# Kernel optimization log

Measured on AMD Instinct MI355X. Metric: run time of the kernel, lower is better.

## Reference

```python
import jax, jax.numpy as jnp
import numpy as np

B, T, C = 4, 2048, 1024
E, I, K = 8, 1408, 2
N_SHARED = 1
IS = I * N_SHARED  # shared expert intermediate size


def setup_inputs() -> dict:
    key = jax.random.key(0)
    ks = jax.random.split(key, 8)
    s = 0.02
    return {
        "x": jax.random.normal(ks[0], (B, T, C), dtype=jnp.float32),
        "Wg": jax.random.normal(ks[1], (E, C), dtype=jnp.float32) * s,   # gate: Linear(C->E), weight [out,in]
        "W1": jax.random.normal(ks[2], (E, I, C), dtype=jnp.float32) * s,  # fc_1 per expert
        "W2": jax.random.normal(ks[3], (E, I, C), dtype=jnp.float32) * s,  # fc_2 per expert
        "W3": jax.random.normal(ks[4], (E, C, I), dtype=jnp.float32) * s,  # proj per expert
        "Ws1": jax.random.normal(ks[5], (IS, C), dtype=jnp.float32) * s,   # shared expert fc_1
        "Ws2": jax.random.normal(ks[6], (IS, C), dtype=jnp.float32) * s,   # shared expert fc_2
        "Ws3": jax.random.normal(ks[7], (C, IS), dtype=jnp.float32) * s,   # shared expert proj
    }


def reference(x, Wg, W1, W2, W3, Ws1, Ws2, Ws3):
    b, t, c = x.shape
    xf = x.reshape(-1, c)                       # [N, C]
    n = xf.shape[0]

    # Router: softmax in float32, top-k gating
    logits = xf @ Wg.T                          # [N, E]
    probs = jax.nn.softmax(logits.astype(jnp.float32), axis=-1)
    topk_p, topk_i = jax.lax.top_k(probs, K)    # [N, K]
    topk_p = topk_p.astype(x.dtype)

    # Dense combine weights: w[n, e] = sum_k topk_p[n, k] * (topk_i[n, k] == e)
    comb = jnp.zeros((n, E), dtype=x.dtype).at[jnp.arange(n)[:, None], topk_i].add(topk_p)

    # All experts on all tokens (dense equivalent of masked dispatch), weighted combine
    g = jnp.einsum('nc,eic->nei', xf, W1)       # [N, E, I]
    u = jnp.einsum('nc,eic->nei', xf, W2)       # [N, E, I]
    h = jax.nn.silu(g) * u                      # SwiGLU
    o = jnp.einsum('nei,eci->nec', h, W3)       # [N, E, C]
    y = jnp.einsum('nec,ne->nc', o, comb).reshape(b, t, c)

    # Shared expert on the residual input
    shared = (jax.nn.silu(x @ Ws1.T) * (x @ Ws2.T)) @ Ws3.T  # [B, T, C]
    return y + shared
```

## Files before the change

kernel.cpp:

```cpp
#include <hip/hip_runtime.h>
#include <stdint.h>

typedef __bf16 bf16;
typedef __attribute__((ext_vector_type(8))) __bf16 bf16x8;
typedef __attribute__((ext_vector_type(4))) float f32x4;

#define N_TOK 8192
#define C_DIM 1024
#define I_DIM 1408
#define NE 8
#define NEA 9
#define H_ROWS 25600

#define CNT_OFF   0
#define OFFS_OFF  64
#define TT_OFF    128
#define BTOK_OFF  192
#define BP_OFF    (BTOK_OFF + NE * N_TOK * 4)
#define ROUTER_END (BP_OFF + NE * N_TOK * 4)
#define TSEL_OFF  ROUTER_END
#define TP0_OFF   (TSEL_OFF + N_TOK * 4)
#define TP1_OFF   (TP0_OFF + N_TOK * 4)
#define XB_OFF    (1u << 20)
#define WB1_OFF   (18u << 20)
#define WB2_OFF   (43u << 20)
#define WB3_OFF   (68u << 20)
#define H_OFF     (93u << 20)

__device__ __forceinline__ void gload16(const void* g, void* l) {
  __builtin_amdgcn_global_load_lds(
      (const __attribute__((address_space(1))) void*)g,
      (__attribute__((address_space(3))) void*)l, 16, 0, 0);
}

__device__ __forceinline__ void vmw(int sel) {
  if (sel == 8) asm volatile("s_waitcnt vmcnt(8)" ::: "memory");
  else asm volatile("s_waitcnt vmcnt(0)" ::: "memory");
}

#define SCHED() __builtin_amdgcn_sched_barrier(0)

#define PHASE(BASE, HALF, READB, STAGEBLK, VMSEL)                              \
  {                                                                            \
    if (READB) {                                                               \
      _Pragma("unroll") for (int nf = 0; nf < 4; ++nf)                         \
          bv[nf] = *(const bf16x8*)((BASE) + 16384 + boff[nf]);                \
    }                                                                          \
    _Pragma("unroll") for (int q = 0; q < 4; ++q)                              \
        av[q] = *(const bf16x8*)((BASE) + aoff[(HALF)*4 + q]);                 \
    STAGEBLK;                                                                  \
    SCHED();                                                                   \
    __builtin_amdgcn_s_barrier();                                              \
    asm volatile("s_waitcnt lgkmcnt(0)" ::: "memory");                         \
    SCHED();                                                                   \
    __builtin_amdgcn_s_setprio(1);                                             \
    _Pragma("unroll") for (int q = 0; q < 4; ++q)                              \
        _Pragma("unroll") for (int nf = 0; nf < 4; ++nf)                       \
            acc[(HALF)*4 + q][nf] = __builtin_amdgcn_mfma_f32_16x16x32_bf16(   \
                av[q], bv[nf], acc[(HALF)*4 + q][nf], 0, 0, 0);                \
    __builtin_amdgcn_s_setprio(0);                                             \
    SCHED();                                                                   \
    if ((VMSEL) >= 0) vmw(VMSEL);                                              \
    __builtin_amdgcn_s_barrier();                                              \
    SCHED();                                                                   \
  }

__global__ __launch_bounds__(256) void convert_kernel(
    const float* __restrict__ src, bf16* __restrict__ dst, int n8) {
  int i = blockIdx.x * 256 + threadIdx.x;
  if (i >= n8) return;
  const float* s = src + (size_t)i * 8;
  float4 a = *(const float4*)(s);
  float4 b = *(const float4*)(s + 4);
  bf16x8 v;
  v[0] = (bf16)a.x; v[1] = (bf16)a.y; v[2] = (bf16)a.z; v[3] = (bf16)a.w;
  v[4] = (bf16)b.x; v[5] = (bf16)b.y; v[6] = (bf16)b.z; v[7] = (bf16)b.w;
  *(bf16x8*)(dst + (size_t)i * 8) = v;
}

__global__ __launch_bounds__(256) void logits_kernel(
    const float* __restrict__ x, const float* __restrict__ Wg,
    int* __restrict__ tsel, float* __restrict__ tp0, float* __restrict__ tp1) {
  __shared__ __align__(16) float wg[NE * C_DIM];
  int t = threadIdx.x;
#pragma unroll
  for (int j = 0; j < 8; ++j) {
    int idx = (t + 256 * j) * 4;
    *(float4*)&wg[idx] = *(const float4*)&Wg[idx];
  }
  __syncthreads();
  int wid = t >> 6, lane = t & 63;
  int tok = blockIdx.x * 4 + wid;
  const float* xr = x + (size_t)tok * C_DIM;
  float acc[NE];
#pragma unroll
  for (int e = 0; e < NE; ++e) acc[e] = 0.f;
#pragma unroll
  for (int j = 0; j < 4; ++j) {
    int c4 = (lane + 64 * j) * 4;
    float4 xv = *(const float4*)&xr[c4];
#pragma unroll
    for (int e = 0; e < NE; ++e) {
      float4 wv = *(const float4*)&wg[e * C_DIM + c4];
      acc[e] += xv.x * wv.x + xv.y * wv.y + xv.z * wv.z + xv.w * wv.w;
    }
  }
  for (int o = 32; o >= 1; o >>= 1)
#pragma unroll
    for (int e = 0; e < NE; ++e) acc[e] += __shfl_xor(acc[e], o, 64);
  if (lane == 0) {
    float m = acc[0];
#pragma unroll
    for (int e = 1; e < NE; ++e) m = fmaxf(m, acc[e]);
    float p[NE], s = 0.f;
#pragma unroll
    for (int e = 0; e < NE; ++e) { p[e] = __expf(acc[e] - m); s += p[e]; }
    float inv = 1.f / s;
#pragma unroll
    for (int e = 0; e < NE; ++e) p[e] *= inv;
    int e0 = 0; float p0 = p[0];
#pragma unroll
    for (int e = 1; e < NE; ++e) if (p[e] > p0) { p0 = p[e]; e0 = e; }
    int e1 = -1; float p1 = -1.f;
#pragma unroll
    for (int e = 0; e < NE; ++e) {
      if (e == e0) continue;
      if (p[e] > p1) { p1 = p[e]; e1 = e; }
    }
    tsel[tok] = e0 | (e1 << 8);
    tp0[tok] = p0;
    tp1[tok] = p1;
  }
}

__global__ __launch_bounds__(1024) void bucketize_kernel(
    const int* __restrict__ tsel, const float* __restrict__ tp0,
    const float* __restrict__ tp1, int* __restrict__ cnt,
    int* __restrict__ btok, float* __restrict__ bp) {
  int e = blockIdx.x;
  int t = threadIdx.x;
  __shared__ int psum[1024];
  int sel[8], loc[8];
  int cntloc = 0;
  int base_tok = t * 8;
#pragma unroll
  for (int j = 0; j < 8; ++j) {
    int s = tsel[base_tok + j];
    int hit = ((s & 0xff) == e) ? 1 : ((((s >> 8) & 0xff) == e) ? 2 : 0);
    sel[j] = hit;
    loc[j] = cntloc;
    cntloc += (hit != 0);
  }
  psum[t] = cntloc;
  __syncthreads();
  for (int off = 1; off < 1024; off <<= 1) {
    int v = (t >= off) ? psum[t - off] : 0;
    __syncthreads();
    psum[t] += v;
    __syncthreads();
  }
  int excl = psum[t] - cntloc;
  if (t == 1023) cnt[e] = psum[1023];
#pragma unroll
  for (int j = 0; j < 8; ++j) {
    if (sel[j]) {
      int pos = excl + loc[j];
      int tok = base_tok + j;
      btok[e * N_TOK + pos] = tok;
      bp[e * N_TOK + pos] = (sel[j] == 1) ? tp0[tok] : tp1[tok];
    }
  }
}

__global__ void offsets_kernel(const int* __restrict__ cnt, int* __restrict__ offs,
                               int* __restrict__ tt) {
  if (threadIdx.x == 0) {
    int a = 0, b = 0;
    for (int e = 0; e < NE; ++e) {
      offs[e] = a; tt[e] = b;
      int pad = (cnt[e] + 127) & ~127;
      a += pad;
      b += (pad + 255) >> 8;
    }
    offs[NE] = a; tt[NE] = b;
  }
}

__device__ __forceinline__ int swz_off(int row, int kg) {
  return row * 64 + ((kg ^ ((row >> 1) & 3)) * 16);
}

__global__ __launch_bounds__(512) void stage1_kernel(
    const bf16* __restrict__ xb, const bf16* __restrict__ wb1,
    const bf16* __restrict__ wb2, const int* __restrict__ cnt,
    const int* __restrict__ offs, const int* __restrict__ tt,
    const int* __restrict__ btok, bf16* __restrict__ H) {
  int bid = blockIdx.x;
  int wgid = (bid & 7) * 154 + (bid >> 3);
  int tau = wgid % 112;
  int i0 = (wgid / 112) * 128;
  int e, row0, slotbase, limit;
  if (tau < 32) {
    e = NE; row0 = tau * 256; slotbase = 0; limit = N_TOK;
  } else {
    int tr = tau - 32;
    if (tr >= tt[NE]) return;
    e = NE - 1;
#pragma unroll
    for (int q = 0; q < NE; ++q) if (tr < tt[q + 1]) { e = q; break; }
    row0 = (tr - tt[e]) * 256;
    slotbase = N_TOK + offs[e];
    limit = cnt[e];
    if (row0 >= limit) return;
  }

  __shared__ __align__(16) char smem[131072];
  const int t = threadIdx.x;
  const int lane = t & 63, wid = t >> 6;
  const int wr = wid >> 2, wc = wid & 3;
  const int l15 = lane & 15, l4 = lane >> 4;

  const int srow = t >> 2;
  const int gsrc = (t & 3) ^ ((srow >> 1) & 3);
  int ar0 = row0 + srow, ar1 = row0 + srow + 128;
  int tok0, tok1;
  if (e == NE) { tok0 = ar0; tok1 = ar1; }
  else {
    int ix0 = e * N_TOK + (ar0 < N_TOK ? ar0 : N_TOK - 1);
    int ix1 = e * N_TOK + (ar1 < N_TOK ? ar1 : N_TOK - 1);
    tok0 = btok[ix0] & (N_TOK - 1);
    tok1 = btok[ix1] & (N_TOK - 1);
  }
  const bf16* asrc0 = xb + (size_t)tok0 * C_DIM + gsrc * 8;
  const bf16* asrc1 = xb + (size_t)tok1 * C_DIM + gsrc * 8;
  const bf16* bsrc0;
  const bf16* bsrc1;
  {
    int r = srow;
    int q = r >> 4, m = q >> 1, sel = q & 1;
    int irow = i0 + m * 16 + (r & 15);
    bsrc0 = (sel ? wb2 : wb1) + ((size_t)e * I_DIM + irow) * C_DIM + gsrc * 8;
    r = srow + 128;
    q = r >> 4; m = q >> 1; sel = q & 1;
    irow = i0 + m * 16 + (r & 15);
    bsrc1 = (sel ? wb2 : wb1) + ((size_t)e * I_DIM + irow) * C_DIM + gsrc * 8;
  }
  const int lo0 = t * 16;
  const int NKT = C_DIM / 32;

  auto stA = [&](int z) {
    if (z < NKT) {
      char* d = smem + (z & 3) * 32768;
      int k = z * 32;
      gload16(asrc0 + k, d + lo0);
      gload16(asrc1 + k, d + 8192 + lo0);
    }
  };
  auto stB = [&](int z) {
    if (z < NKT) {
      char* d = smem + (z & 3) * 32768 + 16384;
      int k = z * 32;
      gload16(bsrc0 + k, d + lo0);
      gload16(bsrc1 + k, d + 8192 + lo0);
    }
  };

  int aoff[8], boff[4];
#pragma unroll
  for (int mf = 0; mf < 8; ++mf) aoff[mf] = swz_off(wr * 128 + mf * 16 + l15, l4);
#pragma unroll
  for (int nf = 0; nf < 4; ++nf) boff[nf] = swz_off(wc * 64 + nf * 16 + l15, l4);

  f32x4 acc[8][4];
  f32x4 zero = {0.f, 0.f, 0.f, 0.f};
#pragma unroll
  for (int mf = 0; mf < 8; ++mf)
#pragma unroll
    for (int nf = 0; nf < 4; ++nf) acc[mf][nf] = zero;
  bf16x8 av[4], bv[4];

  stB(0); stA(0); stB(1); stA(1); stB(2); stA(2);
  asm volatile("s_waitcnt vmcnt(0)" ::: "memory");
  __builtin_amdgcn_s_barrier();
  SCHED();

  const int NIT = NKT / 2;
  for (int it = 0; it < NIT; ++it) {
    char* q0 = smem + ((2 * it) & 3) * 32768;
    char* q1 = smem + ((2 * it + 1) & 3) * 32768;
    int zB = 2 * it + 3, zC = 2 * it + 4;
    int v1 = (zB < NKT) ? 8 : 0;
    int v2 = (zC < NKT) ? 8 : 0;
    PHASE(q0, 0, 1, { stB(zB); }, -1);
    PHASE(q0, 1, 0, { stA(zB); }, v1);
    PHASE(q1, 0, 1, { stB(zC); }, -1);
    PHASE(q1, 1, 0, { stA(zC); }, v2);
  }

#pragma unroll
  for (int mf = 0; mf < 8; ++mf)
#pragma unroll
    for (int r = 0; r < 4; ++r) {
      int rr = row0 + wr * 128 + mf * 16 + l4 * 4 + r;
      if (rr < limit) {
#pragma unroll
        for (int p = 0; p < 2; ++p) {
          float g = acc[mf][2 * p][r];
          float u = acc[mf][2 * p + 1][r];
          float h = (g / (1.f + __expf(-g))) * u;
          int col = i0 + (wc * 2 + p) * 16 + l15;
          H[(size_t)(slotbase + rr) * I_DIM + col] = (bf16)h;
        }
      }
    }
}

template <int SHARED>
__global__ __launch_bounds__(512) void stage2_kernel(
    const bf16* __restrict__ H, const bf16* __restrict__ wb3,
    const int* __restrict__ cnt, const int* __restrict__ offs,
    const int* __restrict__ tt, const int* __restrict__ btok,
    const float* __restrict__ bp, float* __restrict__ y) {
  int bid = blockIdx.x;
  int e, row0, slotbase, limit, c0;
  if (SHARED) {
    int wgid = (bid & 7) * 16 + (bid >> 3);
    e = NE; row0 = (wgid % 32) * 256; slotbase = 0; limit = N_TOK;
    c0 = (wgid / 32) * 256;
  } else {
    int wgid = (bid & 7) * 40 + (bid >> 3);
    int tr = wgid % 80;
    c0 = (wgid / 80) * 256;
    if (tr >= tt[NE]) return;
    e = NE - 1;
#pragma unroll
    for (int q = 0; q < NE; ++q) if (tr < tt[q + 1]) { e = q; break; }
    row0 = (tr - tt[e]) * 256;
    slotbase = N_TOK + offs[e];
    limit = cnt[e];
    if (row0 >= limit) return;
  }

  __shared__ __align__(16) char smem[131072];
  const int t = threadIdx.x;
  const int lane = t & 63, wid = t >> 6;
  const int wr = wid >> 2, wc = wid & 3;
  const int l15 = lane & 15, l4 = lane >> 4;

  const int srow = t >> 2;
  const int gsrc = (t & 3) ^ ((srow >> 1) & 3);
  int sr0 = slotbase + row0 + srow;        if (sr0 > H_ROWS - 1) sr0 = H_ROWS - 1;
  int sr1 = slotbase + row0 + srow + 128;  if (sr1 > H_ROWS - 1) sr1 = H_ROWS - 1;
  const bf16* asrc0 = H + (size_t)sr0 * I_DIM + gsrc * 8;
  const bf16* asrc1 = H + (size_t)sr1 * I_DIM + gsrc * 8;
  const bf16* bsrc0 = wb3 + ((size_t)e * C_DIM + c0 + srow) * I_DIM + gsrc * 8;
  const bf16* bsrc1 = bsrc0 + (size_t)128 * I_DIM;
  const int lo0 = t * 16;
  const int NKT = I_DIM / 32;

  auto stA = [&](int z) {
    if (z < NKT) {
      char* d = smem + (z & 3) * 32768;
      int k = z * 32;
      gload16(asrc0 + k, d + lo0);
      gload16(asrc1 + k, d + 8192 + lo0);
    }
  };
  auto stB = [&](int z) {
    if (z < NKT) {
      char* d = smem + (z & 3) * 32768 + 16384;
      int k = z * 32;
      gload16(bsrc0 + k, d + lo0);
      gload16(bsrc1 + k, d + 8192 + lo0);
    }
  };

  int aoff[8], boff[4];
#pragma unroll
  for (int mf = 0; mf < 8; ++mf) aoff[mf] = swz_off(wr * 128 + mf * 16 + l15, l4);
#pragma unroll
  for (int nf = 0; nf < 4; ++nf) boff[nf] = swz_off(wc * 64 + nf * 16 + l15, l4);

  f32x4 acc[8][4];
  f32x4 zero = {0.f, 0.f, 0.f, 0.f};
#pragma unroll
  for (int mf = 0; mf < 8; ++mf)
#pragma unroll
    for (int nf = 0; nf < 4; ++nf) acc[mf][nf] = zero;
  bf16x8 av[4], bv[4];

  stB(0); stA(0); stB(1); stA(1); stB(2); stA(2);
  asm volatile("s_waitcnt vmcnt(0)" ::: "memory");
  __builtin_amdgcn_s_barrier();
  SCHED();

  const int NIT = NKT / 2;
  for (int it = 0; it < NIT; ++it) {
    char* q0 = smem + ((2 * it) & 3) * 32768;
    char* q1 = smem + ((2 * it + 1) & 3) * 32768;
    int zB = 2 * it + 3, zC = 2 * it + 4;
    int v1 = (zB < NKT) ? 8 : 0;
    int v2 = (zC < NKT) ? 8 : 0;
    PHASE(q0, 0, 1, { stB(zB); }, -1);
    PHASE(q0, 1, 0, { stA(zB); }, v1);
    PHASE(q1, 0, 1, { stB(zC); }, -1);
    PHASE(q1, 1, 0, { stA(zC); }, v2);
  }

#pragma unroll
  for (int mf = 0; mf < 8; ++mf)
#pragma unroll
    for (int r = 0; r < 4; ++r) {
      int idx = row0 + wr * 128 + mf * 16 + l4 * 4 + r;
      if (idx < limit) {
        if (SHARED) {
#pragma unroll
          for (int nf = 0; nf < 4; ++nf) {
            int col = c0 + wc * 64 + nf * 16 + l15;
            y[(size_t)idx * C_DIM + col] = acc[mf][nf][r];
          }
        } else {
          float p = bp[e * N_TOK + idx];
          int tok = btok[e * N_TOK + idx] & (N_TOK - 1);
#pragma unroll
          for (int nf = 0; nf < 4; ++nf) {
            int col = c0 + wc * 64 + nf * 16 + l15;
            atomicAdd(&y[(size_t)tok * C_DIM + col], p * acc[mf][nf][r]);
          }
        }
      }
    }
}

extern "C" void kernel_launch(void* const* d_in, const int* in_sizes, int n_in,
                              void* d_out, int out_size, void* d_ws, size_t ws_size,
                              hipStream_t stream) {
  const float* x = (const float*)d_in[0];
  const float* Wg = (const float*)d_in[1];
  const float* W1 = (const float*)d_in[2];
  const float* W2 = (const float*)d_in[3];
  const float* W3 = (const float*)d_in[4];
  const float* Ws1 = (const float*)d_in[5];
  const float* Ws2 = (const float*)d_in[6];
  const float* Ws3 = (const float*)d_in[7];
  float* y = (float*)d_out;
  char* ws = (char*)d_ws;

  int* cnt = (int*)(ws + CNT_OFF);
  int* offs = (int*)(ws + OFFS_OFF);
  int* tt = (int*)(ws + TT_OFF);
  int* btok = (int*)(ws + BTOK_OFF);
  float* bp = (float*)(ws + BP_OFF);
  int* tsel = (int*)(ws + TSEL_OFF);
  float* tp0 = (float*)(ws + TP0_OFF);
  float* tp1 = (float*)(ws + TP1_OFF);
  bf16* xb = (bf16*)(ws + XB_OFF);
  bf16* wb1 = (bf16*)(ws + WB1_OFF);
  bf16* wb2 = (bf16*)(ws + WB2_OFF);
  bf16* wb3 = (bf16*)(ws + WB3_OFF);
  bf16* H = (bf16*)(ws + H_OFF);

  hipMemsetAsync(ws, 0, ROUTER_END, stream);

  auto conv = [&](const float* s, bf16* d, size_t n) {
    int n8 = (int)(n / 8);
    convert_kernel<<<(n8 + 255) / 256, 256, 0, stream>>>(s, d, n8);
  };
  conv(x, xb, (size_t)N_TOK * C_DIM);
  conv(W1, wb1, (size_t)NE * I_DIM * C_DIM);
  conv(Ws1, wb1 + (size_t)NE * I_DIM * C_DIM, (size_t)I_DIM * C_DIM);
  conv(W2, wb2, (size_t)NE * I_DIM * C_DIM);
  conv(Ws2, wb2 + (size_t)NE * I_DIM * C_DIM, (size_t)I_DIM * C_DIM);
  conv(W3, wb3, (size_t)NE * C_DIM * I_DIM);
  conv(Ws3, wb3 + (size_t)NE * C_DIM * I_DIM, (size_t)C_DIM * I_DIM);

  logits_kernel<<<N_TOK / 4, 256, 0, stream>>>(x, Wg, tsel, tp0, tp1);
  bucketize_kernel<<<NE, 1024, 0, stream>>>(tsel, tp0, tp1, cnt, btok, bp);
  offsets_kernel<<<1, 64, 0, stream>>>(cnt, offs, tt);

  stage1_kernel<<<1232, 512, 0, stream>>>(xb, wb1, wb2, cnt, offs, tt, btok, H);
  stage2_kernel<1><<<128, 512, 0, stream>>>(H, wb3, cnt, offs, tt, btok, bp, y);
  stage2_kernel<0><<<320, 512, 0, stream>>>(H, wb3, cnt, offs, tt, btok, bp, y);
}
```

Before: 416.5 us.

## Double-buffer LDS fragment reads to overlap with MFMA in expert GEMMs

Restructures the inner GEMM loop of both expert kernels so that shared-memory fragment reads for the next phase are issued before the current phase's MFMA block, using ping-pong register buffers (av0/av1, bv0/bv1). This drops the per-phase lgkmcnt(0) wait and halves the barriers per phase, aiming to hide LDS latency behind matrix math. It also changes the vmcnt waits to vmcnt(6) on alternating phases. Costs are higher register pressure from the extra fragment buffers and some risk of LDS read/write ordering hazards if the staged buffers overlap the ones being read.

```diff
diff --git a/kernel.cpp b/kernel.cpp
--- a/kernel.cpp
+++ b/kernel.cpp
@@ -33,36 +33,19 @@
       (__attribute__((address_space(3))) void*)l, 16, 0, 0);
 }
 
-__device__ __forceinline__ void vmw(int sel) {
-  if (sel == 8) asm volatile("s_waitcnt vmcnt(8)" ::: "memory");
-  else asm volatile("s_waitcnt vmcnt(0)" ::: "memory");
-}
-
 #define SCHED() __builtin_amdgcn_sched_barrier(0)
-
-#define PHASE(BASE, HALF, READB, STAGEBLK, VMSEL)                              \
+#define BAR()   __builtin_amdgcn_s_barrier()
+#define VM6()   asm volatile("s_waitcnt vmcnt(6)" ::: "memory")
+#define VM0()   asm volatile("s_waitcnt vmcnt(0)" ::: "memory")
+
+#define MM(AV, BV, H)                                                          \
   {                                                                            \
-    if (READB) {                                                               \
-      _Pragma("unroll") for (int nf = 0; nf < 4; ++nf)                         \
-          bv[nf] = *(const bf16x8*)((BASE) + 16384 + boff[nf]);                \
-    }                                                                          \
-    _Pragma("unroll") for (int q = 0; q < 4; ++q)                              \
-        av[q] = *(const bf16x8*)((BASE) + aoff[(HALF)*4 + q]);                 \
-    STAGEBLK;                                                                  \
-    SCHED();                                                                   \
-    __builtin_amdgcn_s_barrier();                                              \
-    asm volatile("s_waitcnt lgkmcnt(0)" ::: "memory");                         \
-    SCHED();                                                                   \
     __builtin_amdgcn_s_setprio(1);                                             \
     _Pragma("unroll") for (int q = 0; q < 4; ++q)                              \
         _Pragma("unroll") for (int nf = 0; nf < 4; ++nf)                       \
-            acc[(HALF)*4 + q][nf] = __builtin_amdgcn_mfma_f32_16x16x32_bf16(   \
-                av[q], bv[nf], acc[(HALF)*4 + q][nf], 0, 0, 0);                \
+            acc[(H)*4 + q][nf] = __builtin_amdgcn_mfma_f32_16x16x32_bf16(      \
+                AV[q], BV[nf], acc[(H)*4 + q][nf], 0, 0, 0);                   \
     __builtin_amdgcn_s_setprio(0);                                             \
-    SCHED();                                                                   \
-    if ((VMSEL) >= 0) vmw(VMSEL);                                              \
-    __builtin_amdgcn_s_barrier();                                              \
-    SCHED();                                                                   \
   }
 
 __global__ __launch_bounds__(256) void convert_kernel(
@@ -277,25 +260,47 @@
   for (int mf = 0; mf < 8; ++mf)
 #pragma unroll
     for (int nf = 0; nf < 4; ++nf) acc[mf][nf] = zero;
-  bf16x8 av[4], bv[4];
+
+  bf16x8 av0[4], av1[4], bv0[4], bv1[4];
+  auto rdA = [&](bf16x8* dst, int T, int h) {
+    char* base = smem + (T & 3) * 32768;
+#pragma unroll
+    for (int q = 0; q < 4; ++q) dst[q] = *(const bf16x8*)(base + aoff[h * 4 + q]);
+  };
+  auto rdB = [&](bf16x8* dst, int T) {
+    char* base = smem + (T & 3) * 32768 + 16384;
+#pragma unroll
+    for (int nf = 0; nf < 4; ++nf) dst[nf] = *(const bf16x8*)(base + boff[nf]);
+  };
 
   stB(0); stA(0); stB(1); stA(1); stB(2); stA(2);
-  asm volatile("s_waitcnt vmcnt(0)" ::: "memory");
-  __builtin_amdgcn_s_barrier();
+  VM0();
+  BAR();
   SCHED();
+  rdA(av0, 0, 0); rdB(bv0, 0);
 
   const int NIT = NKT / 2;
   for (int it = 0; it < NIT; ++it) {
-    char* q0 = smem + ((2 * it) & 3) * 32768;
-    char* q1 = smem + ((2 * it + 1) & 3) * 32768;
+    int T0 = 2 * it, T1 = 2 * it + 1, T2n = 2 * it + 2;
     int zB = 2 * it + 3, zC = 2 * it + 4;
-    int v1 = (zB < NKT) ? 8 : 0;
-    int v2 = (zC < NKT) ? 8 : 0;
-    PHASE(q0, 0, 1, { stB(zB); }, -1);
-    PHASE(q0, 1, 0, { stA(zB); }, v1);
-    PHASE(q1, 0, 1, { stB(zC); }, -1);
-    PHASE(q1, 1, 0, { stA(zC); }, v2);
-  }
+    rdA(av1, T0, 1);
+    MM(av0, bv0, 0);
+    stB(zB);
+    SCHED(); VM6(); BAR(); SCHED();
+    rdA(av0, T1, 0); rdB(bv1, T1);
+    MM(av1, bv0, 1);
+    stA(zB);
+    SCHED(); BAR(); SCHED();
+    rdA(av1, T1, 1);
+    MM(av0, bv1, 0);
+    stB(zC);
+    SCHED(); VM6(); BAR(); SCHED();
+    if (it + 1 < NIT) { rdA(av0, T2n, 0); rdB(bv0, T2n); }
+    MM(av1, bv1, 1);
+    stA(zC);
+    SCHED(); BAR(); SCHED();
+  }
+  VM0();
 
 #pragma unroll
   for (int mf = 0; mf < 8; ++mf)
@@ -387,25 +392,47 @@
   for (int mf = 0; mf < 8; ++mf)
 #pragma unroll
     for (int nf = 0; nf < 4; ++nf) acc[mf][nf] = zero;
-  bf16x8 av[4], bv[4];
+
+  bf16x8 av0[4], av1[4], bv0[4], bv1[4];
+  auto rdA = [&](bf16x8* dst, int T, int h) {
+    char* base = smem + (T & 3) * 32768;
+#pragma unroll
+    for (int q = 0; q < 4; ++q) dst[q] = *(const bf16x8*)(base + aoff[h * 4 + q]);
+  };
+  auto rdB = [&](bf16x8* dst, int T) {
+    char* base = smem + (T & 3) * 32768 + 16384;
+#pragma unroll
+    for (int nf = 0; nf < 4; ++nf) dst[nf] = *(const bf16x8*)(base + boff[nf]);
+  };
 
   stB(0); stA(0); stB(1); stA(1); stB(2); stA(2);
-  asm volatile("s_waitcnt vmcnt(0)" ::: "memory");
-  __builtin_amdgcn_s_barrier();
+  VM0();
+  BAR();
   SCHED();
+  rdA(av0, 0, 0); rdB(bv0, 0);
 
   const int NIT = NKT / 2;
   for (int it = 0; it < NIT; ++it) {
-    char* q0 = smem + ((2 * it) & 3) * 32768;
-    char* q1 = smem + ((2 * it + 1) & 3) * 32768;
+    int T0 = 2 * it, T1 = 2 * it + 1, T2n = 2 * it + 2;
     int zB = 2 * it + 3, zC = 2 * it + 4;
-    int v1 = (zB < NKT) ? 8 : 0;
-    int v2 = (zC < NKT) ? 8 : 0;
-    PHASE(q0, 0, 1, { stB(zB); }, -1);
-    PHASE(q0, 1, 0, { stA(zB); }, v1);
-    PHASE(q1, 0, 1, { stB(zC); }, -1);
-    PHASE(q1, 1, 0, { stA(zC); }, v2);
-  }
+    rdA(av1, T0, 1);
+    MM(av0, bv0, 0);
+    stB(zB);
+    SCHED(); VM6(); BAR(); SCHED();
+    rdA(av0, T1, 0); rdB(bv1, T1);
+    MM(av1, bv0, 1);
+    stA(zB);
+    SCHED(); BAR(); SCHED();
+    rdA(av1, T1, 1);
+    MM(av0, bv1, 0);
+    stB(zC);
+    SCHED(); VM6(); BAR(); SCHED();
+    if (it + 1 < NIT) { rdA(av0, T2n, 0); rdB(bv0, T2n); }
+    MM(av1, bv1, 1);
+    stA(zC);
+    SCHED(); BAR(); SCHED();
+  }
+  VM0();
 
 #pragma unroll
   for (int mf = 0; mf < 8; ++mf)
```

Result: faster. 407.4 us (-2.2%).

## Restructure MoE GEMM pipelines into two 64-wide K buffers with finer staging

Applied to the files above, without the earlier changes.

Both the fused gate/up expert GEMM and the down-projection GEMM switch from four 32-wide K slots to two 64 KB buffers, each holding a 64-wide K tile split into two halves. The main loop now runs eight phases per iteration, interleaving A/B half-tile loads with MFMA work and waiting with vmcnt(6) instead of 8. This is meant to reduce barrier and wait stalls and keep more loads in flight per compute step. The more intricate wait accounting risks races or a changed load-to-compute distance. The down projection has 22 K tiles (I_DIM/64), so each iteration covers two of them.

```diff
diff --git a/kernel.cpp b/kernel.cpp
--- a/kernel.cpp
+++ b/kernel.cpp
@@ -33,35 +33,38 @@
       (__attribute__((address_space(3))) void*)l, 16, 0, 0);
 }
 
+#define SCHED() __builtin_amdgcn_sched_barrier(0)
+#define BAR()   __builtin_amdgcn_s_barrier()
+
 __device__ __forceinline__ void vmw(int sel) {
-  if (sel == 8) asm volatile("s_waitcnt vmcnt(8)" ::: "memory");
-  else asm volatile("s_waitcnt vmcnt(0)" ::: "memory");
-}
-
-#define SCHED() __builtin_amdgcn_sched_barrier(0)
-
-#define PHASE(BASE, HALF, READB, STAGEBLK, VMSEL)                              \
+  if (sel == 6) asm volatile("s_waitcnt vmcnt(6)" ::: "memory");
+  else if (sel == 0) asm volatile("s_waitcnt vmcnt(0)" ::: "memory");
+}
+
+#define PH(BUF, S, H_, READB, STAGEBLK, VMSEL)                                 \
   {                                                                            \
+    char* ab = smem + (BUF) * 65536 + (S) * 16384;                             \
+    char* bb = smem + (BUF) * 65536 + 32768 + (S) * 16384;                     \
     if (READB) {                                                               \
       _Pragma("unroll") for (int nf = 0; nf < 4; ++nf)                         \
-          bv[nf] = *(const bf16x8*)((BASE) + 16384 + boff[nf]);                \
+          bv[nf] = *(const bf16x8*)(bb + boff[nf]);                            \
     }                                                                          \
     _Pragma("unroll") for (int q = 0; q < 4; ++q)                              \
-        av[q] = *(const bf16x8*)((BASE) + aoff[(HALF)*4 + q]);                 \
+        av[q] = *(const bf16x8*)(ab + aoff[(H_)*4 + q]);                       \
     STAGEBLK;                                                                  \
     SCHED();                                                                   \
-    __builtin_amdgcn_s_barrier();                                              \
+    BAR();                                                                     \
     asm volatile("s_waitcnt lgkmcnt(0)" ::: "memory");                         \
     SCHED();                                                                   \
     __builtin_amdgcn_s_setprio(1);                                             \
     _Pragma("unroll") for (int q = 0; q < 4; ++q)                              \
         _Pragma("unroll") for (int nf = 0; nf < 4; ++nf)                       \
-            acc[(HALF)*4 + q][nf] = __builtin_amdgcn_mfma_f32_16x16x32_bf16(   \
-                av[q], bv[nf], acc[(HALF)*4 + q][nf], 0, 0, 0);                \
+            acc[(H_)*4 + q][nf] = __builtin_amdgcn_mfma_f32_16x16x32_bf16(     \
+                av[q], bv[nf], acc[(H_)*4 + q][nf], 0, 0, 0);                  \
     __builtin_amdgcn_s_setprio(0);                                             \
     SCHED();                                                                   \
-    if ((VMSEL) >= 0) vmw(VMSEL);                                              \
-    __builtin_amdgcn_s_barrier();                                              \
+    vmw(VMSEL);                                                                \
+    BAR();                                                                     \
     SCHED();                                                                   \
   }
 
@@ -246,20 +249,20 @@
     bsrc1 = (sel ? wb2 : wb1) + ((size_t)e * I_DIM + irow) * C_DIM + gsrc * 8;
   }
   const int lo0 = t * 16;
-  const int NKT = C_DIM / 32;
-
-  auto stA = [&](int z) {
+  const int NKT = C_DIM / 64;
+
+  auto stA = [&](int z, int s) {
     if (z < NKT) {
-      char* d = smem + (z & 3) * 32768;
-      int k = z * 32;
+      char* d = smem + (z & 1) * 65536 + s * 16384;
+      int k = z * 64 + s * 32;
       gload16(asrc0 + k, d + lo0);
       gload16(asrc1 + k, d + 8192 + lo0);
     }
   };
-  auto stB = [&](int z) {
+  auto stB = [&](int z, int s) {
     if (z < NKT) {
-      char* d = smem + (z & 3) * 32768 + 16384;
-      int k = z * 32;
+      char* d = smem + (z & 1) * 65536 + 32768 + s * 16384;
+      int k = z * 64 + s * 32;
       gload16(bsrc0 + k, d + lo0);
       gload16(bsrc1 + k, d + 8192 + lo0);
     }
@@ -279,23 +282,27 @@
     for (int nf = 0; nf < 4; ++nf) acc[mf][nf] = zero;
   bf16x8 av[4], bv[4];
 
-  stB(0); stA(0); stB(1); stA(1); stB(2); stA(2);
-  asm volatile("s_waitcnt vmcnt(0)" ::: "memory");
-  __builtin_amdgcn_s_barrier();
+  stB(0, 0); stA(0, 0); stB(0, 1); stA(0, 1);
+  stB(1, 0); stA(1, 0); stB(1, 1);
   SCHED();
+  asm volatile("s_waitcnt vmcnt(6)" ::: "memory");
+  BAR(); SCHED();
 
   const int NIT = NKT / 2;
   for (int it = 0; it < NIT; ++it) {
-    char* q0 = smem + ((2 * it) & 3) * 32768;
-    char* q1 = smem + ((2 * it + 1) & 3) * 32768;
-    int zB = 2 * it + 3, zC = 2 * it + 4;
-    int v1 = (zB < NKT) ? 8 : 0;
-    int v2 = (zC < NKT) ? 8 : 0;
-    PHASE(q0, 0, 1, { stB(zB); }, -1);
-    PHASE(q0, 1, 0, { stA(zB); }, v1);
-    PHASE(q1, 0, 1, { stB(zC); }, -1);
-    PHASE(q1, 1, 0, { stA(zC); }, v2);
-  }
+    int T1z = 2 * it + 1, T2z = 2 * it + 2, T3z = 2 * it + 3;
+    int vm4 = (it == NIT - 1) ? 0 : 6;
+    int vm8 = (it == NIT - 1) ? -1 : 6;
+    PH(0, 0, 0, 1, { stA(T1z, 1); }, -1);
+    PH(0, 0, 1, 0, { stB(T2z, 0); }, -1);
+    PH(0, 1, 0, 1, { stA(T2z, 0); }, -1);
+    PH(0, 1, 1, 0, { stB(T2z, 1); }, vm4);
+    PH(1, 0, 0, 1, { stA(T2z, 1); }, -1);
+    PH(1, 0, 1, 0, { stB(T3z, 0); }, -1);
+    PH(1, 1, 0, 1, { stA(T3z, 0); }, -1);
+    PH(1, 1, 1, 0, { stB(T3z, 1); }, vm8);
+  }
+  asm volatile("s_waitcnt vmcnt(0)" ::: "memory");
 
 #pragma unroll
   for (int mf = 0; mf < 8; ++mf)
@@ -356,20 +363,20 @@
   const bf16* bsrc0 = wb3 + ((size_t)e * C_DIM + c0 + srow) * I_DIM + gsrc * 8;
   const bf16* bsrc1 = bsrc0 + (size_t)128 * I_DIM;
   const int lo0 = t * 16;
-  const int NKT = I_DIM / 32;
-
-  auto stA = [&](int z) {
+  const int NKT = I_DIM / 64;
+
+  auto stA = [&](int z, int s) {
     if (z < NKT) {
-      char* d = smem + (z & 3) * 32768;
-      int k = z * 32;
+      char* d = smem + (z & 1) * 65536 + s * 16384;
+      int k = z * 64 + s * 32;
       gload16(asrc0 + k, d + lo0);
       gload16(asrc1 + k, d + 8192 + lo0);
     }
   };
-  auto stB = [&](int z) {
+  auto stB = [&](int z, int s) {
     if (z < NKT) {
-      char* d = smem + (z & 3) * 32768 + 16384;
-      int k = z * 32;
+      char* d = smem + (z & 1) * 65536 + 32768 + s * 16384;
+      int k = z * 64 + s * 32;
       gload16(bsrc0 + k, d + lo0);
       gload16(bsrc1 + k, d + 8192 + lo0);
     }
@@ -389,23 +396,27 @@
     for (int nf = 0; nf < 4; ++nf) acc[mf][nf] = zero;
   bf16x8 av[4], bv[4];
 
-  stB(0); stA(0); stB(1); stA(1); stB(2); stA(2);
-  asm volatile("s_waitcnt vmcnt(0)" ::: "memory");
-  __builtin_amdgcn_s_barrier();
+  stB(0, 0); stA(0, 0); stB(0, 1); stA(0, 1);
+  stB(1, 0); stA(1, 0); stB(1, 1);
   SCHED();
+  asm volatile("s_waitcnt vmcnt(6)" ::: "memory");
+  BAR(); SCHED();
 
   const int NIT = NKT / 2;
   for (int it = 0; it < NIT; ++it) {
-    char* q0 = smem + ((2 * it) & 3) * 32768;
-    char* q1 = smem + ((2 * it + 1) & 3) * 32768;
-    int zB = 2 * it + 3, zC = 2 * it + 4;
-    int v1 = (zB < NKT) ? 8 : 0;
-    int v2 = (zC < NKT) ? 8 : 0;
-    PHASE(q0, 0, 1, { stB(zB); }, -1);
-    PHASE(q0, 1, 0, { stA(zB); }, v1);
-    PHASE(q1, 0, 1, { stB(zC); }, -1);
-    PHASE(q1, 1, 0, { stA(zC); }, v2);
-  }
+    int T1z = 2 * it + 1, T2z = 2 * it + 2, T3z = 2 * it + 3;
+    int vm4 = (it == NIT - 1) ? 0 : 6;
+    int vm8 = (it == NIT - 1) ? -1 : 6;
+    PH(0, 0, 0, 1, { stA(T1z, 1); }, -1);
+    PH(0, 0, 1, 0, { stB(T2z, 0); }, -1);
+    PH(0, 1, 0, 1, { stA(T2z, 0); }, -1);
+    PH(0, 1, 1, 0, { stB(T2z, 1); }, vm4);
+    PH(1, 0, 0, 1, { stA(T2z, 1); }, -1);
+    PH(1, 0, 1, 0, { stB(T3z, 0); }, -1);
+    PH(1, 1, 0, 1, { stA(T3z, 0); }, -1);
+    PH(1, 1, 1, 0, { stB(T3z, 1); }, vm8);
+  }
+  asm volatile("s_waitcnt vmcnt(0)" ::: "memory");
 
 #pragma unroll
   for (int mf = 0; mf < 8; ++mf)
```

New measurement: 410.0 us. About the same (-1.6%).
